# Optimization experiments

Hardware: AMD Instinct MI355X
Metric: run time of the kernel (lower is better)

Reference implementation:

```python
import jax, jax.numpy as jnp
import numpy as np

NUM_INPUTS = 256
NUM_OUTPUTS = 256
NUM_MID_LAYERS = 15  # num_layers=16 -> 1 first + 15 middle + 1 output layer
N = 16384            # num_neurons_per_layer
W = 4096             # bitarray width (parallel evaluations)


def setup_inputs() -> dict:
    key = jax.random.key(0)
    k0, k1, k2, k3, k4, k5, k6 = jax.random.split(key, 7)
    input_bits = jax.random.randint(k0, (NUM_INPUTS, W), 0, 2).astype(jnp.bool_)
    idx0 = jax.random.randint(k1, (N, 2), 0, NUM_INPUTS, dtype=jnp.int32)
    idx_mid = jax.random.randint(k2, (NUM_MID_LAYERS, N, 2), 0, N, dtype=jnp.int32)
    idx_out = jax.random.randint(k3, (NUM_OUTPUTS, 2), 0, N, dtype=jnp.int32)
    nor0 = jax.random.randint(k4, (N,), 0, 2).astype(jnp.bool_)
    nor_mid = jax.random.randint(k5, (NUM_MID_LAYERS, N), 0, 2).astype(jnp.bool_)
    nor_out = jax.random.randint(k6, (NUM_OUTPUTS,), 0, 2).astype(jnp.bool_)
    return {"input_bits": input_bits, "idx0": idx0, "idx_mid": idx_mid,
            "idx_out": idx_out, "nor0": nor0, "nor_mid": nor_mid, "nor_out": nor_out}


def _nand_layer(x, idx, nor):
    # x: [num_in, W] bool; idx: [num_out, 2]; nor: [num_out]
    a = x[idx[:, 0]]  # [num_out, W]
    b = x[idx[:, 1]]
    # NOT(where(nor, a|b, a&b))  == per-node NOR or NAND
    return ~jnp.where(nor[:, None], a | b, a & b)


def reference(input_bits, idx0, idx_mid, idx_out, nor0, nor_mid, nor_out):
    x = _nand_layer(input_bits, idx0, nor0)  # [N, W]

    def step(x, layer):
        idx, nor = layer
        return _nand_layer(x, idx, nor), None

    x, _ = jax.lax.scan(step, x, (idx_mid, nor_mid))
    out = _nand_layer(x, idx_out, nor_out)  # [NUM_OUTPUTS, W]
    return out
```

## Files before the change

kernel.cpp:

```cpp
#include <hip/hip_runtime.h>
#include <stdint.h>

#define N_GATES   16384
#define NUM_IN    256
#define NUM_OUT   256
#define MID_LAYERS 15
#define W         4096
#define BLOCK     1024
#define WG_COLS   32
#define NUM_WG    (W / WG_COLS)

__global__ __launch_bounds__(BLOCK)
void nand_graph_kernel(const uint32_t* __restrict__ input_bits,
                       const int2*     __restrict__ idx0,
                       const int2*     __restrict__ idx_mid,
                       const int2*     __restrict__ idx_out,
                       const uint32_t* __restrict__ nor0,
                       const uint32_t* __restrict__ nor_mid,
                       const uint32_t* __restrict__ nor_out,
                       int*            __restrict__ out)
{
    extern __shared__ uint32_t lds[];
    uint32_t* bufA = lds;
    uint32_t* bufB = lds + N_GATES;
    uint32_t* wrd  = lds + 2 * N_GATES;

    const int wg   = blockIdx.x;
    const int tid  = threadIdx.x;
    const int lane = tid & 63;
    const int wave = tid >> 6;
    const int colbase = wg * WG_COLS;

    for (int r2 = wave; r2 < NUM_IN / 2; r2 += BLOCK / 64) {
        int r = r2 * 2 + (lane >> 5);
        int c = lane & 31;
        uint32_t v = input_bits[r * W + colbase + c];
        unsigned long long m = __ballot(v != 0u);
        if ((lane & 31) == 0) {
            wrd[r] = (uint32_t)(m >> ((lane >> 5) * 32));
        }
    }
    __syncthreads();

    for (int g = tid; g < N_GATES; g += BLOCK) {
        int2 ix = idx0[g];
        uint32_t a = wrd[ix.x];
        uint32_t b = wrd[ix.y];
        uint32_t nn = nor0[g];
        bufA[g] = ~(nn ? (a | b) : (a & b));
    }
    __syncthreads();

    uint32_t* cur = bufA;
    uint32_t* nxt = bufB;
    for (int l = 0; l < MID_LAYERS; ++l) {
        const int2*     idx = idx_mid + (size_t)l * N_GATES;
        const uint32_t* nor = nor_mid + (size_t)l * N_GATES;
        for (int g = tid; g < N_GATES; g += BLOCK) {
            int2 ix = idx[g];
            uint32_t a = cur[ix.x];
            uint32_t b = cur[ix.y];
            uint32_t nn = nor[g];
            nxt[g] = ~(nn ? (a | b) : (a & b));
        }
        __syncthreads();
        uint32_t* t = cur; cur = nxt; nxt = t;
    }

    if (tid < NUM_OUT) {
        int2 ix = idx_out[tid];
        uint32_t a = cur[ix.x];
        uint32_t b = cur[ix.y];
        uint32_t nn = nor_out[tid];
        wrd[tid] = ~(nn ? (a | b) : (a & b));
    }
    __syncthreads();

    for (int r2 = wave; r2 < NUM_OUT / 2; r2 += BLOCK / 64) {
        int r = r2 * 2 + (lane >> 5);
        int c = lane & 31;
        uint32_t bits = wrd[r];
        out[r * W + colbase + c] = (int)((bits >> c) & 1u);
    }
}

extern "C" void kernel_launch(void* const* d_in, const int* in_sizes, int n_in,
                              void* d_out, int out_size, void* d_ws, size_t ws_size,
                              hipStream_t stream) {
    const uint32_t* input_bits = (const uint32_t*)d_in[0];
    const int2*     idx0       = (const int2*)d_in[1];
    const int2*     idx_mid    = (const int2*)d_in[2];
    const int2*     idx_out    = (const int2*)d_in[3];
    const uint32_t* nor0       = (const uint32_t*)d_in[4];
    const uint32_t* nor_mid    = (const uint32_t*)d_in[5];
    const uint32_t* nor_out    = (const uint32_t*)d_in[6];
    int*            out        = (int*)d_out;

    const size_t lds_bytes = (size_t)(2 * N_GATES + 256) * sizeof(uint32_t);

    hipFuncSetAttribute(reinterpret_cast<const void*>(nand_graph_kernel),
                        hipFuncAttributeMaxDynamicSharedMemorySize, (int)lds_bytes);

    nand_graph_kernel<<<dim3(NUM_WG), dim3(BLOCK), lds_bytes, stream>>>(
        input_bits, idx0, idx_mid, idx_out, nor0, nor_mid, nor_out, out);
}
```

Before: 54.35 us.

## Use 16-bit words, halve LDS, prefetch next layer's indices into registers

Each workgroup now packs 16 columns into a uint16 word instead of 32 columns into a uint32, which halves LDS usage and doubles the number of workgroups. Launch bounds ask for two 1024-thread blocks per CU. Gate indices and nor flags are read as int4 vectors into registers, and the next layer's values are prefetched before the barrier so global load latency overlaps the sync. Outputs are written as packed 64-bit stores. In exchange, the per-lane bit width is halved, so twice as many workgroups each re-read the full index and nor arrays, roughly doubling global traffic for that metadata.

```diff
diff --git a/kernel.cpp b/kernel.cpp
--- a/kernel.cpp
+++ b/kernel.cpp
@@ -1,86 +1,120 @@
 #include <hip/hip_runtime.h>
 #include <stdint.h>
 
-#define N_GATES   16384
-#define NUM_IN    256
-#define NUM_OUT   256
+#define N_GATES    16384
+#define NUM_IN     256
+#define NUM_OUT    256
 #define MID_LAYERS 15
-#define W         4096
-#define BLOCK     1024
-#define WG_COLS   32
-#define NUM_WG    (W / WG_COLS)
+#define W          4096
+#define BLOCK      1024
+#define WG_COLS    16
+#define NUM_WG     (W / WG_COLS)
+#define QPT        (N_GATES / (4 * BLOCK))
 
-__global__ __launch_bounds__(BLOCK)
+__global__ __launch_bounds__(BLOCK, 2)
 void nand_graph_kernel(const uint32_t* __restrict__ input_bits,
-                       const int2*     __restrict__ idx0,
-                       const int2*     __restrict__ idx_mid,
+                       const int4*     __restrict__ idx0_4,
+                       const int4*     __restrict__ idx_mid_4,
                        const int2*     __restrict__ idx_out,
-                       const uint32_t* __restrict__ nor0,
-                       const uint32_t* __restrict__ nor_mid,
+                       const int4*     __restrict__ nor0_4,
+                       const int4*     __restrict__ nor_mid_4,
                        const uint32_t* __restrict__ nor_out,
                        int*            __restrict__ out)
 {
-    extern __shared__ uint32_t lds[];
-    uint32_t* bufA = lds;
-    uint32_t* bufB = lds + N_GATES;
-    uint32_t* wrd  = lds + 2 * N_GATES;
+    extern __shared__ __align__(16) uint16_t lds16[];
+    uint16_t* bufA = lds16;
+    uint16_t* bufB = lds16 + N_GATES;
+    uint16_t* wrd  = lds16 + 2 * N_GATES;
 
-    const int wg   = blockIdx.x;
-    const int tid  = threadIdx.x;
-    const int lane = tid & 63;
-    const int wave = tid >> 6;
-    const int colbase = wg * WG_COLS;
+    const int tid     = threadIdx.x;
+    const int lane    = tid & 63;
+    const int wave    = tid >> 6;
+    const int colbase = blockIdx.x * WG_COLS;
 
-    for (int r2 = wave; r2 < NUM_IN / 2; r2 += BLOCK / 64) {
-        int r = r2 * 2 + (lane >> 5);
-        int c = lane & 31;
+    int4 ixA[QPT], ixB[QPT], nnq[QPT];
+
+    #pragma unroll
+    for (int q = 0; q < QPT; ++q) {
+        int Q = tid + q * BLOCK;
+        ixA[q] = idx0_4[2 * Q];
+        ixB[q] = idx0_4[2 * Q + 1];
+        nnq[q] = nor0_4[Q];
+    }
+
+    #pragma unroll
+    for (int it = wave; it < NUM_IN / 4; it += BLOCK / 64) {
+        int r = it * 4 + (lane >> 4);
+        int c = lane & 15;
         uint32_t v = input_bits[r * W + colbase + c];
         unsigned long long m = __ballot(v != 0u);
-        if ((lane & 31) == 0) {
-            wrd[r] = (uint32_t)(m >> ((lane >> 5) * 32));
+        if ((lane & 15) == 0)
+            wrd[r] = (uint16_t)(m >> ((lane >> 4) * 16));
+    }
+    __syncthreads();
+
+    auto run_gates = [&](const uint16_t* __restrict__ src, uint16_t* __restrict__ dst) {
+        #pragma unroll
+        for (int q = 0; q < QPT; ++q) {
+            int Q = tid + q * BLOCK;
+            uint32_t a0 = src[ixA[q].x], b0 = src[ixA[q].y];
+            uint32_t a1 = src[ixA[q].z], b1 = src[ixA[q].w];
+            uint32_t a2 = src[ixB[q].x], b2 = src[ixB[q].y];
+            uint32_t a3 = src[ixB[q].z], b3 = src[ixB[q].w];
+            uint32_t r0 = ~(nnq[q].x ? (a0 | b0) : (a0 & b0));
+            uint32_t r1 = ~(nnq[q].y ? (a1 | b1) : (a1 & b1));
+            uint32_t r2 = ~(nnq[q].z ? (a2 | b2) : (a2 & b2));
+            uint32_t r3 = ~(nnq[q].w ? (a3 | b3) : (a3 & b3));
+            uint32_t lo = (r0 & 0xFFFFu) | (r1 << 16);
+            uint32_t hi = (r2 & 0xFFFFu) | (r3 << 16);
+            *reinterpret_cast<uint2*>(dst + 4 * Q) = make_uint2(lo, hi);
+        }
+    };
+
+    run_gates(wrd, bufA);
+    {
+        const int4* i4 = idx_mid_4;
+        const int4* n4 = nor_mid_4;
+        #pragma unroll
+        for (int q = 0; q < QPT; ++q) {
+            int Q = tid + q * BLOCK;
+            ixA[q] = i4[2 * Q];
+            ixB[q] = i4[2 * Q + 1];
+            nnq[q] = n4[Q];
         }
     }
     __syncthreads();
 
-    for (int g = tid; g < N_GATES; g += BLOCK) {
-        int2 ix = idx0[g];
-        uint32_t a = wrd[ix.x];
-        uint32_t b = wrd[ix.y];
-        uint32_t nn = nor0[g];
-        bufA[g] = ~(nn ? (a | b) : (a & b));
-    }
-    __syncthreads();
-
-    uint32_t* cur = bufA;
-    uint32_t* nxt = bufB;
+    uint16_t* cur = bufA;
+    uint16_t* nxt = bufB;
     for (int l = 0; l < MID_LAYERS; ++l) {
-        const int2*     idx = idx_mid + (size_t)l * N_GATES;
-        const uint32_t* nor = nor_mid + (size_t)l * N_GATES;
-        for (int g = tid; g < N_GATES; g += BLOCK) {
-            int2 ix = idx[g];
-            uint32_t a = cur[ix.x];
-            uint32_t b = cur[ix.y];
-            uint32_t nn = nor[g];
-            nxt[g] = ~(nn ? (a | b) : (a & b));
+        run_gates(cur, nxt);
+        if (l + 1 < MID_LAYERS) {
+            const int4* i4 = idx_mid_4 + (size_t)(l + 1) * (N_GATES / 2);
+            const int4* n4 = nor_mid_4 + (size_t)(l + 1) * (N_GATES / 4);
+            #pragma unroll
+            for (int q = 0; q < QPT; ++q) {
+                int Q = tid + q * BLOCK;
+                ixA[q] = i4[2 * Q];
+                ixB[q] = i4[2 * Q + 1];
+                nnq[q] = n4[Q];
+            }
         }
         __syncthreads();
-        uint32_t* t = cur; cur = nxt; nxt = t;
+        uint16_t* t = cur; cur = nxt; nxt = t;
     }
 
     if (tid < NUM_OUT) {
         int2 ix = idx_out[tid];
         uint32_t a = cur[ix.x];
         uint32_t b = cur[ix.y];
-        uint32_t nn = nor_out[tid];
-        wrd[tid] = ~(nn ? (a | b) : (a & b));
+        wrd[tid] = (uint16_t)~(nor_out[tid] ? (a | b) : (a & b));
     }
     __syncthreads();
 
-    for (int r2 = wave; r2 < NUM_OUT / 2; r2 += BLOCK / 64) {
-        int r = r2 * 2 + (lane >> 5);
-        int c = lane & 31;
-        uint32_t bits = wrd[r];
-        out[r * W + colbase + c] = (int)((bits >> c) & 1u);
+    #pragma unroll
+    for (int i = tid; i < NUM_OUT * WG_COLS; i += BLOCK) {
+        int r = i >> 4, c = i & 15;
+        out[r * W + colbase + c] = (int)((wrd[r] >> c) & 1u);
     }
 }
 
@@ -88,19 +122,19 @@
                               void* d_out, int out_size, void* d_ws, size_t ws_size,
                               hipStream_t stream) {
     const uint32_t* input_bits = (const uint32_t*)d_in[0];
-    const int2*     idx0       = (const int2*)d_in[1];
-    const int2*     idx_mid    = (const int2*)d_in[2];
+    const int4*     idx0_4     = (const int4*)d_in[1];
+    const int4*     idx_mid_4  = (const int4*)d_in[2];
     const int2*     idx_out    = (const int2*)d_in[3];
-    const uint32_t* nor0       = (const uint32_t*)d_in[4];
-    const uint32_t* nor_mid    = (const uint32_t*)d_in[5];
+    const int4*     nor0_4     = (const int4*)d_in[4];
+    const int4*     nor_mid_4  = (const int4*)d_in[5];
     const uint32_t* nor_out    = (const uint32_t*)d_in[6];
     int*            out        = (int*)d_out;
 
-    const size_t lds_bytes = (size_t)(2 * N_GATES + 256) * sizeof(uint32_t);
+    const size_t lds_bytes = (size_t)(2 * N_GATES + 256) * sizeof(uint16_t);
 
     hipFuncSetAttribute(reinterpret_cast<const void*>(nand_graph_kernel),
                         hipFuncAttributeMaxDynamicSharedMemorySize, (int)lds_bytes);
 
     nand_graph_kernel<<<dim3(NUM_WG), dim3(BLOCK), lds_bytes, stream>>>(
-        input_bits, idx0, idx_mid, idx_out, nor0, nor_mid, nor_out, out);
+        input_bits, idx0_4, idx_mid_4, idx_out, nor0_4, nor_mid_4, nor_out, out);
 }
```

Result: faster. 43.73 us (-19.5%).
